# Kernel optimization log

Hardware: AMD Instinct MI355X
Metric: run time of the kernel (lower is better)

## Reference

```python
import jax, jax.numpy as jnp
import numpy as np

B, S, D, H = 4, 2048, 1024, 16
DK = D // H

def setup_inputs() -> dict:
    key = jax.random.key(0)
    ks = jax.random.split(key, 8)
    q = jax.random.normal(ks[0], (B, S, D), dtype=jnp.float32)
    k = jax.random.normal(ks[1], (B, S, D), dtype=jnp.float32)
    v = jax.random.normal(ks[2], (B, S, D), dtype=jnp.float32)
    # broadcastable causal mask [1,1,S,S]; 0 -> masked
    mask = jnp.tril(jnp.ones((S, S), dtype=jnp.int32))[None, None]
    sc = 1.0 / np.sqrt(D)
    w_q = jax.random.normal(ks[3], (D, D), dtype=jnp.float32) * sc
    w_k = jax.random.normal(ks[4], (D, D), dtype=jnp.float32) * sc
    w_v = jax.random.normal(ks[5], (D, D), dtype=jnp.float32) * sc
    w_o = jax.random.normal(ks[6], (D, D), dtype=jnp.float32) * sc
    return {"q": q, "k": k, "v": v, "mask": mask,
            "w_q": w_q, "w_k": w_k, "w_v": w_v, "w_o": w_o}


def reference(q, k, v, mask, w_q, w_k, w_v, w_o):
    # Linear (no bias): x @ W^T, torch convention
    def proj(x, w):
        return jnp.einsum('bsd,ed->bse', x, w)
    # [B,S,D] -> [B,H,S,DK]
    def split_heads(x):
        return x.reshape(B, S, H, DK).transpose(0, 2, 1, 3)

    query = split_heads(proj(q, w_q))
    key_ = split_heads(proj(k, w_k))
    value = split_heads(proj(v, w_v))

    scores = jnp.einsum('bhqd,bhkd->bhqk', query, key_) / jnp.sqrt(
        jnp.asarray(DK, dtype=query.dtype))
    scores = jnp.where(mask == 0, jnp.asarray(-1e9, dtype=scores.dtype), scores)
    attn = jax.nn.softmax(scores, axis=-1)  # dropout p=0.0 -> identity
    x = jnp.einsum('bhqk,bhkd->bhqd', attn, value)
    x = x.transpose(0, 2, 1, 3).reshape(B, S, D)
    return jnp.einsum('bsd,ed->bse', x, w_o)
```

## Files before the change

kernel.cpp:

```cpp
#include <hip/hip_runtime.h>
#include <hip/hip_bf16.h>

#define B_ 4
#define S_ 2048
#define D_ 1024
#define H_ 16
#define DK_ 64

typedef unsigned short u16;
typedef __bf16 bf16x8 __attribute__((ext_vector_type(8)));
typedef float f32x4 __attribute__((ext_vector_type(4)));

typedef const unsigned int __attribute__((address_space(1))) guint;
typedef unsigned int __attribute__((address_space(3))) luint;

__device__ __forceinline__ void gld16(const u16* g, u16* l) {
  __builtin_amdgcn_global_load_lds((guint*)g, (luint*)l, 16, 0, 0);
}

__device__ __forceinline__ u16 f2b(float f) {
  __hip_bfloat16 h = __float2bfloat16(f);
  return __builtin_bit_cast(u16, h);
}
__device__ __forceinline__ ushort4 f2b4(float4 f) {
  ushort4 r;
  r.x = f2b(f.x); r.y = f2b(f.y); r.z = f2b(f.z); r.w = f2b(f.w);
  return r;
}
__device__ __forceinline__ bf16x8 ldb8(const u16* p) {
  union { uint4 u; bf16x8 v; } x;
  x.u = *(const uint4*)p;
  return x.v;
}

struct CvtAllArgs {
  const float* s[7];
  u16* d[7];
};
__global__ __launch_bounds__(256) void cvt_all(CvtAllArgs a) {
  const int z = blockIdx.y;
  const int bx = blockIdx.x;
  const float* s;
  u16* d;
  int i;
  if (z < 3) {
    s = a.s[z]; d = a.d[z];
    i = bx * 256 + threadIdx.x;
  } else {
    if (bx >= 2048) return;
    const int wsel = bx >> 9;
    s = a.s[3 + wsel]; d = a.d[3 + wsel];
    i = (bx & 511) * 256 + threadIdx.x;
  }
  float4 x = ((const float4*)s)[2 * i];
  float4 y = ((const float4*)s)[2 * i + 1];
  ((ushort4*)d)[2 * i] = f2b4(x);
  ((ushort4*)d)[2 * i + 1] = f2b4(y);
}

__device__ __forceinline__ void swz_bnbm(int& bn, int& bm) {
  const int id2 = blockIdx.y * 8 + blockIdx.x;
  const int wg = (id2 & 7) * 64 + (id2 >> 3);
  bn = wg & 7;
  bm = wg >> 3;
}

template <bool OUT_QKV>
__device__ __forceinline__ void gemm_body(const u16* __restrict__ A,
                                          const u16* __restrict__ W,
                                          void* __restrict__ C, float scale) {
  constexpr int K = D_;
  __shared__ u16 As[128 * 32];
  __shared__ u16 Ws[128 * 32];
  const int t = threadIdx.x;
  const int lane = t & 63, w = t >> 6;
  const int quad = lane >> 4, m16 = lane & 15;
  int bn, bm;
  swz_bnbm(bn, bm);
  const int wm = (w >> 1) * 64, wn = (w & 1) * 64;
  const int sr = lane >> 2, sc8 = (lane & 3) * 8;

  f32x4 acc[4][4];
  const f32x4 zero = {0.f, 0.f, 0.f, 0.f};
#pragma unroll
  for (int i = 0; i < 4; i++)
#pragma unroll
    for (int j = 0; j < 4; j++) acc[i][j] = zero;

  const u16* Ag = A + (size_t)(bm * 128 + w * 32 + sr) * K + sc8;
  const u16* Wg = W + (size_t)(bn * 128 + w * 32 + sr) * K + sc8;
  u16* AsB = &As[w * 1024];
  u16* WsB = &Ws[w * 1024];

  for (int k0 = 0; k0 < K; k0 += 32) {
    __syncthreads();
    gld16(Ag + k0, AsB);
    gld16(Ag + (size_t)16 * K + k0, AsB + 512);
    gld16(Wg + k0, WsB);
    gld16(Wg + (size_t)16 * K + k0, WsB + 512);
    __syncthreads();

    bf16x8 af[4], wf[4];
#pragma unroll
    for (int mt = 0; mt < 4; mt++)
      af[mt] = ldb8(&As[(wm + mt * 16 + m16) * 32 + quad * 8]);
#pragma unroll
    for (int nt = 0; nt < 4; nt++)
      wf[nt] = ldb8(&Ws[(wn + nt * 16 + m16) * 32 + quad * 8]);
#pragma unroll
    for (int mt = 0; mt < 4; mt++)
#pragma unroll
      for (int nt = 0; nt < 4; nt++)
        acc[mt][nt] = __builtin_amdgcn_mfma_f32_16x16x32_bf16(af[mt], wf[nt],
                                                              acc[mt][nt], 0, 0, 0);
  }

#pragma unroll
  for (int mt = 0; mt < 4; mt++) {
#pragma unroll
    for (int r = 0; r < 4; r++) {
      int m = bm * 128 + wm + mt * 16 + quad * 4 + r;
#pragma unroll
      for (int nt = 0; nt < 4; nt++) {
        int n = bn * 128 + wn + nt * 16 + m16;
        float val = acc[mt][nt][r] * scale;
        if (OUT_QKV) {
          int b = m >> 11, s = m & (S_ - 1);
          int h = n >> 6, dk = n & 63;
          ((u16*)C)[(((size_t)b * H_ + h) * S_ + s) * DK_ + dk] = f2b(val);
        } else {
          ((float*)C)[(size_t)m * D_ + n] = val;
        }
      }
    }
  }
}

struct GemmQkvArgs {
  const u16 *a0, *a1, *a2;
  const u16 *w0, *w1, *w2;
  u16 *c0, *c1, *c2;
  float qscale;
};
__global__ __launch_bounds__(256) void gemm_qkv(GemmQkvArgs g) {
  const int z = blockIdx.z;
  const u16* A = z == 0 ? g.a0 : z == 1 ? g.a1 : g.a2;
  const u16* W = z == 0 ? g.w0 : z == 1 ? g.w1 : g.w2;
  u16* C = z == 0 ? g.c0 : z == 1 ? g.c1 : g.c2;
  gemm_body<true>(A, W, C, z == 0 ? g.qscale : 1.0f);
}

__global__ __launch_bounds__(256) void gemm_o(const u16* __restrict__ A,
                                              const u16* __restrict__ W,
                                              float* __restrict__ C) {
  gemm_body<false>(A, W, C, 1.0f);
}

__global__ __launch_bounds__(256) void transpose_v(const u16* __restrict__ Vp,
                                                   u16* __restrict__ VpT) {
  constexpr int LDT = 72;
  __shared__ u16 T[64 * LDT];
  const int t = threadIdx.x;
  const int s0 = blockIdx.x * 64, bh = blockIdx.y;
  const size_t base = (size_t)bh * S_ * DK_;
  const int rot = t & 7;
#pragma unroll
  for (int i = 0; i < 2; i++) {
    int c = t + i * 256, row = c >> 3, c8 = (c & 7) * 8;
    union { uint4 u; u16 s[8]; } uv;
    uv.u = *(const uint4*)(Vp + base + (size_t)(s0 + row) * DK_ + c8);
#pragma unroll
    for (int j0 = 0; j0 < 8; j0++) {
      int j = (j0 + rot) & 7;
      T[(c8 + j) * LDT + row] = uv.s[j];
    }
  }
  __syncthreads();
#pragma unroll
  for (int i = 0; i < 2; i++) {
    int c = t + i * 256, row = c >> 3, c8 = (c & 7) * 8;
    uint4 val = *(const uint4*)&T[row * LDT + c8];
    *(uint4*)(VpT + base + (size_t)row * S_ + s0 + c8) = val;
  }
}

__global__ __launch_bounds__(512, 4) void flash_attn(const u16* __restrict__ Qp,
                                                     const u16* __restrict__ Kp,
                                                     const u16* __restrict__ VpT,
                                                     u16* __restrict__ Xb) {
  constexpr int LDK = 72;
  __shared__ u16 Ks[2][64 * LDK];
  __shared__ u16 Vt[2][64 * LDK];
  __shared__ u16 Ps[8][16 * LDK];
  const int t = threadIdx.x;
  const int lane = t & 63, w = t >> 6;
  const int quad = lane >> 4, m16 = lane & 15;
  const int id = blockIdx.x;
  const int g = (id >> 3) & 7;
  const int bh = (id & 7) * 8 + (id >> 6);
  const int b = bh >> 4, h = bh & (H_ - 1);
  const size_t base = (size_t)bh * S_ * DK_;
  const int srow = t >> 3, sc8 = (t & 7) * 8;
  const f32x4 zero = {0.f, 0.f, 0.f, 0.f};

#pragma unroll 1
  for (int pi = 0; pi < 2; pi++) {
    const int qt = pi ? (15 - g) : g;
    const int q0 = qt * 128;
    const int nT = 2 * qt + 2;

    const int qrow = q0 + w * 16 + m16;
    bf16x8 qf0 = ldb8(Qp + base + (size_t)qrow * DK_ + quad * 8);
    bf16x8 qf1 = ldb8(Qp + base + (size_t)qrow * DK_ + 32 + quad * 8);

    f32x4 acc[4];
#pragma unroll
    for (int i = 0; i < 4; i++) acc[i] = zero;
    float rsum[4] = {0.f, 0.f, 0.f, 0.f};

    uint4 kr = *(const uint4*)(Kp + base + (size_t)srow * DK_ + sc8);
    uint4 vr = *(const uint4*)(VpT + base + (size_t)srow * S_ + sc8);

#pragma unroll 1
    for (int ti = 0; ti < nT; ti++) {
      const int kt0 = ti * 64;
      const int cur = ti & 1;
      *(uint4*)&Ks[cur][srow * LDK + sc8] = kr;
      *(uint4*)&Vt[cur][srow * LDK + sc8] = vr;
      __syncthreads();
      if (ti + 1 < nT) {
        kr = *(const uint4*)(Kp + base + (size_t)(kt0 + 64 + srow) * DK_ + sc8);
        vr = *(const uint4*)(VpT + base + (size_t)srow * S_ + kt0 + 64 + sc8);
      }
      const u16* Kc = Ks[cur];
      const u16* Vc = Vt[cur];

      f32x4 sc[4];
      __builtin_amdgcn_s_setprio(1);
#pragma unroll
      for (int nt = 0; nt < 4; nt++) {
        bf16x8 kf0 = ldb8(&Kc[(nt * 16 + m16) * LDK + quad * 8]);
        bf16x8 kf1 = ldb8(&Kc[(nt * 16 + m16) * LDK + 32 + quad * 8]);
        sc[nt] = __builtin_amdgcn_mfma_f32_16x16x32_bf16(kf0, qf0, zero, 0, 0, 0);
        sc[nt] = __builtin_amdgcn_mfma_f32_16x16x32_bf16(kf1, qf1, sc[nt], 0, 0, 0);
      }
      __builtin_amdgcn_s_setprio(0);

      if (ti >= nT - 2) {
        const int qcol = q0 + w * 16 + m16;
#pragma unroll
        for (int nt = 0; nt < 4; nt++) {
          int kg = kt0 + nt * 16 + quad * 4;
#pragma unroll
          for (int r = 0; r < 4; r++)
            if (kg + r > qcol) sc[nt][r] = -1e30f;
        }
      }

      u16* Pw = &Ps[w][0];
#pragma unroll
      for (int nt = 0; nt < 4; nt++) {
        ushort4 pk;
        float p0 = __builtin_amdgcn_exp2f(sc[nt][0]);
        float p1 = __builtin_amdgcn_exp2f(sc[nt][1]);
        float p2 = __builtin_amdgcn_exp2f(sc[nt][2]);
        float p3 = __builtin_amdgcn_exp2f(sc[nt][3]);
        rsum[nt] += (p0 + p1) + (p2 + p3);
        pk.x = f2b(p0); pk.y = f2b(p1); pk.z = f2b(p2); pk.w = f2b(p3);
        *(ushort4*)&Pw[m16 * LDK + nt * 16 + quad * 4] = pk;
      }

      __builtin_amdgcn_s_setprio(1);
#pragma unroll
      for (int s2 = 0; s2 < 2; s2++) {
        bf16x8 pf = ldb8(&Pw[m16 * LDK + s2 * 32 + quad * 8]);
#pragma unroll
        for (int nt = 0; nt < 4; nt++) {
          bf16x8 vf = ldb8(&Vc[(nt * 16 + m16) * LDK + s2 * 32 + quad * 8]);
          acc[nt] = __builtin_amdgcn_mfma_f32_16x16x32_bf16(pf, vf, acc[nt], 0, 0, 0);
        }
      }
      __builtin_amdgcn_s_setprio(0);
    }

    float tot = (rsum[0] + rsum[1]) + (rsum[2] + rsum[3]);
    tot += __shfl_xor(tot, 16);
    tot += __shfl_xor(tot, 32);
    float rcv[4];
#pragma unroll
    for (int r = 0; r < 4; r++)
      rcv[r] = __builtin_amdgcn_rcpf(__shfl(tot, quad * 4 + r, 16));
#pragma unroll
    for (int nt = 0; nt < 4; nt++)
#pragma unroll
      for (int r = 0; r < 4; r++) {
        int rg = q0 + w * 16 + quad * 4 + r;
        Xb[((size_t)b * S_ + rg) * D_ + h * DK_ + nt * 16 + m16] =
            f2b(acc[nt][r] * rcv[r]);
      }
  }
}

extern "C" void kernel_launch(void* const* d_in, const int* in_sizes, int n_in,
                              void* d_out, int out_size, void* d_ws, size_t ws_size,
                              hipStream_t stream) {
  (void)in_sizes; (void)n_in; (void)out_size; (void)ws_size;
  const float* q = (const float*)d_in[0];
  const float* k = (const float*)d_in[1];
  const float* v = (const float*)d_in[2];
  const float* wq = (const float*)d_in[4];
  const float* wk = (const float*)d_in[5];
  const float* wv = (const float*)d_in[6];
  const float* wo = (const float*)d_in[7];

  const size_t nBSD = (size_t)B_ * S_ * D_;
  const size_t nDD = (size_t)D_ * D_;
  u16* ab = (u16*)d_ws;
  u16* wqb = ab + nBSD;
  u16* wkb = wqb + nDD;
  u16* wvb = wkb + nDD;
  u16* wob = wvb + nDD;
  u16* Qp = wob + nDD;
  u16* Kp = Qp + nBSD;
  u16* Vp = Kp + nBSD;
  u16* VpT = ab;
  u16* Xb = Vp;
  u16* abk = (u16*)d_out;
  u16* abv = abk + nBSD;

  const float qscale = 0.125f * 1.44269504089f;

  CvtAllArgs ca = {{q, k, v, wq, wk, wv, wo}, {ab, abk, abv, wqb, wkb, wvb, wob}};
  cvt_all<<<dim3(nBSD / 2048, 4), 256, 0, stream>>>(ca);

  GemmQkvArgs gq = {ab, abk, abv, wqb, wkb, wvb, Qp, Kp, Vp, qscale};
  gemm_qkv<<<dim3(D_ / 128, (B_ * S_) / 128, 3), 256, 0, stream>>>(gq);

  transpose_v<<<dim3(S_ / 64, B_ * H_), 256, 0, stream>>>(Vp, VpT);
  flash_attn<<<512, 512, 0, stream>>>(Qp, Kp, VpT, Xb);

  gemm_o<<<dim3(D_ / 128, (B_ * S_) / 128), 256, 0, stream>>>(Xb, wob, (float*)d_out);
}
```

Measured before the change: 326.8 us.

## Rewrite projection GEMMs as 128x256 tiles with double-buffered LDS; split attention blocks

The projection and output GEMMs become 512-thread kernels with 128x256 tiles, a BK=64 double-buffered LDS pipeline using direct global-to-LDS loads, XOR swizzling and explicit vmcnt waits and barriers. This targets the low reuse and exposed load latency of the old 128x128, BK=32 loop, which synchronised twice per step. Flash attention now runs one query tile per block over 1024 blocks, longest tiles first, with a swizzled P buffer and a higher occupancy hint. The hand-written wait counts and barriers are fragile, and the larger tiles launch fewer blocks.

```diff
diff --git a/kernel.cpp b/kernel.cpp
--- a/kernel.cpp
+++ b/kernel.cpp
@@ -58,27 +58,58 @@
   ((ushort4*)d)[2 * i + 1] = f2b4(y);
 }
 
-__device__ __forceinline__ void swz_bnbm(int& bn, int& bm) {
-  const int id2 = blockIdx.y * 8 + blockIdx.x;
-  const int wg = (id2 & 7) * 64 + (id2 >> 3);
-  bn = wg & 7;
-  bm = wg >> 3;
-}
+#define PRIO1 __builtin_amdgcn_s_setprio(1)
+#define PRIO0 __builtin_amdgcn_s_setprio(0)
+#define BAR __builtin_amdgcn_s_barrier()
+
+#define STG_A(b, tt)                                                          \
+  do {                                                                        \
+    gld16(Ag + (size_t)(tt) * 64, &As[(b) * 8192 + w * 512]);                 \
+    gld16(Ag + (size_t)64 * K + (tt) * 64, &As[(b) * 8192 + 4096 + w * 512]); \
+  } while (0)
+#define STG_B(b, tt)                                                          \
+  do {                                                                        \
+    gld16(Wg + (size_t)(tt) * 64, &Bs[(b) * 16384 + w * 512]);                \
+    gld16(Wg + (size_t)64 * K + (tt) * 64, &Bs[(b) * 16384 + 4096 + w * 512]);\
+    gld16(Wg + (size_t)128 * K + (tt) * 64, &Bs[(b) * 16384 + 8192 + w * 512]);\
+    gld16(Wg + (size_t)192 * K + (tt) * 64, &Bs[(b) * 16384 + 12288 + w * 512]);\
+  } while (0)
+#define MM_HALF(mlo)                                                          \
+  do {                                                                        \
+    _Pragma("unroll") for (int mi_ = (mlo); mi_ < (mlo) + 2; mi_++)           \
+        _Pragma("unroll") for (int ni_ = 0; ni_ < 4; ni_++)                   \
+            _Pragma("unroll") for (int ks_ = 0; ks_ < 2; ks_++)               \
+                acc[mi_][ni_] = __builtin_amdgcn_mfma_f32_16x16x32_bf16(      \
+                    aA[mi_ * 2 + ks_], bB[ni_ * 2 + ks_], acc[mi_][ni_], 0, 0, 0); \
+  } while (0)
 
 template <bool OUT_QKV>
-__device__ __forceinline__ void gemm_body(const u16* __restrict__ A,
-                                          const u16* __restrict__ W,
-                                          void* __restrict__ C, float scale) {
+__device__ __forceinline__ void gemm4_body(const u16* __restrict__ A,
+                                           const u16* __restrict__ W,
+                                           void* __restrict__ C, float scale,
+                                           int bm, int bn) {
   constexpr int K = D_;
-  __shared__ u16 As[128 * 32];
-  __shared__ u16 Ws[128 * 32];
+  constexpr int NI = 8;
+  __shared__ u16 As[2 * 8192];
+  __shared__ u16 Bs[2 * 16384];
   const int t = threadIdx.x;
-  const int lane = t & 63, w = t >> 6;
-  const int quad = lane >> 4, m16 = lane & 15;
-  int bn, bm;
-  swz_bnbm(bn, bm);
-  const int wm = (w >> 1) * 64, wn = (w & 1) * 64;
-  const int sr = lane >> 2, sc8 = (lane & 3) * 8;
+  const int l = t & 63, w = t >> 6;
+  const int quad = l >> 4, m16 = l & 15;
+  const int wm = w >> 2, wn = w & 3;
+  const int lr = l >> 3;
+  const int swz = (m16 & 7) << 3;
+
+  const u16* Ag = A + (size_t)(bm * 128 + w * 8 + lr) * K + ((l & 7) ^ lr) * 8;
+  const u16* Wg = W + (size_t)(bn * 256 + w * 8 + lr) * K + ((l & 7) ^ lr) * 8;
+
+  int au[8], bu[8];
+#pragma unroll
+  for (int i = 0; i < 4; i++)
+#pragma unroll
+    for (int ks = 0; ks < 2; ks++) {
+      au[i * 2 + ks] = ((wm * 64 + i * 16 + m16) * 64 + ks * 32 + quad * 8) ^ swz;
+      bu[i * 2 + ks] = ((wn * 64 + i * 16 + m16) * 64 + ks * 32 + quad * 8) ^ swz;
+    }
 
   f32x4 acc[4][4];
   const f32x4 zero = {0.f, 0.f, 0.f, 0.f};
@@ -87,43 +118,52 @@
 #pragma unroll
     for (int j = 0; j < 4; j++) acc[i][j] = zero;
 
-  const u16* Ag = A + (size_t)(bm * 128 + w * 32 + sr) * K + sc8;
-  const u16* Wg = W + (size_t)(bn * 128 + w * 32 + sr) * K + sc8;
-  u16* AsB = &As[w * 1024];
-  u16* WsB = &Ws[w * 1024];
-
-  for (int k0 = 0; k0 < K; k0 += 32) {
-    __syncthreads();
-    gld16(Ag + k0, AsB);
-    gld16(Ag + (size_t)16 * K + k0, AsB + 512);
-    gld16(Wg + k0, WsB);
-    gld16(Wg + (size_t)16 * K + k0, WsB + 512);
-    __syncthreads();
-
-    bf16x8 af[4], wf[4];
-#pragma unroll
-    for (int mt = 0; mt < 4; mt++)
-      af[mt] = ldb8(&As[(wm + mt * 16 + m16) * 32 + quad * 8]);
-#pragma unroll
-    for (int nt = 0; nt < 4; nt++)
-      wf[nt] = ldb8(&Ws[(wn + nt * 16 + m16) * 32 + quad * 8]);
-#pragma unroll
-    for (int mt = 0; mt < 4; mt++)
-#pragma unroll
-      for (int nt = 0; nt < 4; nt++)
-        acc[mt][nt] = __builtin_amdgcn_mfma_f32_16x16x32_bf16(af[mt], wf[nt],
-                                                              acc[mt][nt], 0, 0, 0);
-  }
-
-#pragma unroll
-  for (int mt = 0; mt < 4; mt++) {
+  bf16x8 aA[8], bB[8];
+
+  STG_A(0, 0); STG_B(0, 0);
+  STG_A(1, 1); STG_B(1, 1);
+  asm volatile("s_waitcnt vmcnt(6)" ::: "memory");
+  __builtin_amdgcn_sched_barrier(0);
+  BAR;
+
+#pragma unroll 1
+  for (int j = 0; j < NI; j++) {
+    const bool st = (j + 1 < NI);
+#pragma unroll
+    for (int i = 0; i < 8; i++) aA[i] = ldb8(&As[au[i]]);
+#pragma unroll
+    for (int i = 0; i < 8; i++) bB[i] = ldb8(&Bs[bu[i]]);
+    BAR; PRIO1; MM_HALF(0); PRIO0; BAR;
+    if (st) {
+      STG_A(0, 2 * j + 2); STG_B(0, 2 * j + 2);
+      asm volatile("s_waitcnt vmcnt(6)" ::: "memory");
+    } else {
+      asm volatile("s_waitcnt vmcnt(0)" ::: "memory");
+    }
+    __builtin_amdgcn_sched_barrier(0);
+    BAR; PRIO1; MM_HALF(2); PRIO0; BAR;
+#pragma unroll
+    for (int i = 0; i < 8; i++) aA[i] = ldb8(&As[8192 + au[i]]);
+#pragma unroll
+    for (int i = 0; i < 8; i++) bB[i] = ldb8(&Bs[16384 + bu[i]]);
+    BAR; PRIO1; MM_HALF(0); PRIO0; BAR;
+    if (st) {
+      STG_A(1, 2 * j + 3); STG_B(1, 2 * j + 3);
+      asm volatile("s_waitcnt vmcnt(6)" ::: "memory");
+    }
+    __builtin_amdgcn_sched_barrier(0);
+    BAR; PRIO1; MM_HALF(2); PRIO0; BAR;
+  }
+
+#pragma unroll
+  for (int mi = 0; mi < 4; mi++) {
 #pragma unroll
     for (int r = 0; r < 4; r++) {
-      int m = bm * 128 + wm + mt * 16 + quad * 4 + r;
-#pragma unroll
-      for (int nt = 0; nt < 4; nt++) {
-        int n = bn * 128 + wn + nt * 16 + m16;
-        float val = acc[mt][nt][r] * scale;
+      int m = bm * 128 + wm * 64 + mi * 16 + quad * 4 + r;
+#pragma unroll
+      for (int ni = 0; ni < 4; ni++) {
+        int n = bn * 256 + wn * 64 + ni * 16 + m16;
+        float val = acc[mi][ni][r] * scale;
         if (OUT_QKV) {
           int b = m >> 11, s = m & (S_ - 1);
           int h = n >> 6, dk = n & 63;
@@ -142,18 +182,24 @@
   u16 *c0, *c1, *c2;
   float qscale;
 };
-__global__ __launch_bounds__(256) void gemm_qkv(GemmQkvArgs g) {
-  const int z = blockIdx.z;
-  const u16* A = z == 0 ? g.a0 : z == 1 ? g.a1 : g.a2;
-  const u16* W = z == 0 ? g.w0 : z == 1 ? g.w1 : g.w2;
-  u16* C = z == 0 ? g.c0 : z == 1 ? g.c1 : g.c2;
-  gemm_body<true>(A, W, C, z == 0 ? g.qscale : 1.0f);
-}
-
-__global__ __launch_bounds__(256) void gemm_o(const u16* __restrict__ A,
-                                              const u16* __restrict__ W,
-                                              float* __restrict__ C) {
-  gemm_body<false>(A, W, C, 1.0f);
+__global__ __launch_bounds__(512, 2) void gemm_qkv4(GemmQkvArgs g) {
+  const int id3 = (blockIdx.z * 64 + blockIdx.y) * 4 + blockIdx.x;
+  const int wg = (id3 & 7) * 96 + (id3 >> 3);
+  const int zz = wg >> 8, rem = wg & 255;
+  const int bm = rem >> 2, bn = rem & 3;
+  const u16* A = zz == 0 ? g.a0 : zz == 1 ? g.a1 : g.a2;
+  const u16* W = zz == 0 ? g.w0 : zz == 1 ? g.w1 : g.w2;
+  u16* C = zz == 0 ? g.c0 : zz == 1 ? g.c1 : g.c2;
+  gemm4_body<true>(A, W, C, zz == 0 ? g.qscale : 1.0f, bm, bn);
+}
+
+__global__ __launch_bounds__(512, 2) void gemm_o(const u16* __restrict__ A,
+                                                 const u16* __restrict__ W,
+                                                 float* __restrict__ C) {
+  const int id2 = blockIdx.y * 4 + blockIdx.x;
+  const int wg = (id2 & 7) * 32 + (id2 >> 3);
+  const int bm = wg >> 2, bn = wg & 3;
+  gemm4_body<false>(A, W, C, 1.0f, bm, bn);
 }
 
 __global__ __launch_bounds__(256) void transpose_v(const u16* __restrict__ Vp,
@@ -184,121 +230,118 @@
   }
 }
 
-__global__ __launch_bounds__(512, 4) void flash_attn(const u16* __restrict__ Qp,
+__global__ __launch_bounds__(512, 6) void flash_attn(const u16* __restrict__ Qp,
                                                      const u16* __restrict__ Kp,
                                                      const u16* __restrict__ VpT,
                                                      u16* __restrict__ Xb) {
   constexpr int LDK = 72;
   __shared__ u16 Ks[2][64 * LDK];
   __shared__ u16 Vt[2][64 * LDK];
-  __shared__ u16 Ps[8][16 * LDK];
+  __shared__ u16 Ps[8][1024];
   const int t = threadIdx.x;
   const int lane = t & 63, w = t >> 6;
   const int quad = lane >> 4, m16 = lane & 15;
   const int id = blockIdx.x;
-  const int g = (id >> 3) & 7;
-  const int bh = (id & 7) * 8 + (id >> 6);
+  const int qt = 15 - (id >> 6);
+  const int bh = id & 63;
   const int b = bh >> 4, h = bh & (H_ - 1);
   const size_t base = (size_t)bh * S_ * DK_;
   const int srow = t >> 3, sc8 = (t & 7) * 8;
+  const int psw = (m16 & 7) << 3;
   const f32x4 zero = {0.f, 0.f, 0.f, 0.f};
 
+  const int q0 = qt * 128;
+  const int nT = 2 * qt + 2;
+
+  const int qrow = q0 + w * 16 + m16;
+  bf16x8 qf0 = ldb8(Qp + base + (size_t)qrow * DK_ + quad * 8);
+  bf16x8 qf1 = ldb8(Qp + base + (size_t)qrow * DK_ + 32 + quad * 8);
+
+  f32x4 acc[4];
+#pragma unroll
+  for (int i = 0; i < 4; i++) acc[i] = zero;
+  float rsum[4] = {0.f, 0.f, 0.f, 0.f};
+
+  uint4 kr = *(const uint4*)(Kp + base + (size_t)srow * DK_ + sc8);
+  uint4 vr = *(const uint4*)(VpT + base + (size_t)srow * S_ + sc8);
+
 #pragma unroll 1
-  for (int pi = 0; pi < 2; pi++) {
-    const int qt = pi ? (15 - g) : g;
-    const int q0 = qt * 128;
-    const int nT = 2 * qt + 2;
-
-    const int qrow = q0 + w * 16 + m16;
-    bf16x8 qf0 = ldb8(Qp + base + (size_t)qrow * DK_ + quad * 8);
-    bf16x8 qf1 = ldb8(Qp + base + (size_t)qrow * DK_ + 32 + quad * 8);
-
-    f32x4 acc[4];
-#pragma unroll
-    for (int i = 0; i < 4; i++) acc[i] = zero;
-    float rsum[4] = {0.f, 0.f, 0.f, 0.f};
-
-    uint4 kr = *(const uint4*)(Kp + base + (size_t)srow * DK_ + sc8);
-    uint4 vr = *(const uint4*)(VpT + base + (size_t)srow * S_ + sc8);
-
-#pragma unroll 1
-    for (int ti = 0; ti < nT; ti++) {
-      const int kt0 = ti * 64;
-      const int cur = ti & 1;
-      *(uint4*)&Ks[cur][srow * LDK + sc8] = kr;
-      *(uint4*)&Vt[cur][srow * LDK + sc8] = vr;
-      __syncthreads();
-      if (ti + 1 < nT) {
-        kr = *(const uint4*)(Kp + base + (size_t)(kt0 + 64 + srow) * DK_ + sc8);
-        vr = *(const uint4*)(VpT + base + (size_t)srow * S_ + kt0 + 64 + sc8);
+  for (int ti = 0; ti < nT; ti++) {
+    const int kt0 = ti * 64;
+    const int cur = ti & 1;
+    *(uint4*)&Ks[cur][srow * LDK + sc8] = kr;
+    *(uint4*)&Vt[cur][srow * LDK + sc8] = vr;
+    __syncthreads();
+    if (ti + 1 < nT) {
+      kr = *(const uint4*)(Kp + base + (size_t)(kt0 + 64 + srow) * DK_ + sc8);
+      vr = *(const uint4*)(VpT + base + (size_t)srow * S_ + kt0 + 64 + sc8);
+    }
+    const u16* Kc = Ks[cur];
+    const u16* Vc = Vt[cur];
+
+    f32x4 sc[4];
+    __builtin_amdgcn_s_setprio(1);
+#pragma unroll
+    for (int nt = 0; nt < 4; nt++) {
+      bf16x8 kf0 = ldb8(&Kc[(nt * 16 + m16) * LDK + quad * 8]);
+      bf16x8 kf1 = ldb8(&Kc[(nt * 16 + m16) * LDK + 32 + quad * 8]);
+      sc[nt] = __builtin_amdgcn_mfma_f32_16x16x32_bf16(kf0, qf0, zero, 0, 0, 0);
+      sc[nt] = __builtin_amdgcn_mfma_f32_16x16x32_bf16(kf1, qf1, sc[nt], 0, 0, 0);
+    }
+    __builtin_amdgcn_s_setprio(0);
+
+    if (ti >= nT - 2) {
+      const int qcol = q0 + w * 16 + m16;
+#pragma unroll
+      for (int nt = 0; nt < 4; nt++) {
+        int kg = kt0 + nt * 16 + quad * 4;
+#pragma unroll
+        for (int r = 0; r < 4; r++)
+          if (kg + r > qcol) sc[nt][r] = -1e30f;
       }
-      const u16* Kc = Ks[cur];
-      const u16* Vc = Vt[cur];
-
-      f32x4 sc[4];
-      __builtin_amdgcn_s_setprio(1);
+    }
+
+    u16* Pw = &Ps[w][0];
+#pragma unroll
+    for (int nt = 0; nt < 4; nt++) {
+      ushort4 pk;
+      float p0 = __builtin_amdgcn_exp2f(sc[nt][0]);
+      float p1 = __builtin_amdgcn_exp2f(sc[nt][1]);
+      float p2 = __builtin_amdgcn_exp2f(sc[nt][2]);
+      float p3 = __builtin_amdgcn_exp2f(sc[nt][3]);
+      rsum[nt] += (p0 + p1) + (p2 + p3);
+      pk.x = f2b(p0); pk.y = f2b(p1); pk.z = f2b(p2); pk.w = f2b(p3);
+      *(ushort4*)&Pw[(m16 * 64 + nt * 16 + quad * 4) ^ psw] = pk;
+    }
+
+    __builtin_amdgcn_s_setprio(1);
+#pragma unroll
+    for (int s2 = 0; s2 < 2; s2++) {
+      bf16x8 pf = ldb8(&Pw[(m16 * 64 + s2 * 32 + quad * 8) ^ psw]);
 #pragma unroll
       for (int nt = 0; nt < 4; nt++) {
-        bf16x8 kf0 = ldb8(&Kc[(nt * 16 + m16) * LDK + quad * 8]);
-        bf16x8 kf1 = ldb8(&Kc[(nt * 16 + m16) * LDK + 32 + quad * 8]);
-        sc[nt] = __builtin_amdgcn_mfma_f32_16x16x32_bf16(kf0, qf0, zero, 0, 0, 0);
-        sc[nt] = __builtin_amdgcn_mfma_f32_16x16x32_bf16(kf1, qf1, sc[nt], 0, 0, 0);
+        bf16x8 vf = ldb8(&Vc[(nt * 16 + m16) * LDK + s2 * 32 + quad * 8]);
+        acc[nt] = __builtin_amdgcn_mfma_f32_16x16x32_bf16(pf, vf, acc[nt], 0, 0, 0);
       }
-      __builtin_amdgcn_s_setprio(0);
-
-      if (ti >= nT - 2) {
-        const int qcol = q0 + w * 16 + m16;
-#pragma unroll
-        for (int nt = 0; nt < 4; nt++) {
-          int kg = kt0 + nt * 16 + quad * 4;
-#pragma unroll
-          for (int r = 0; r < 4; r++)
-            if (kg + r > qcol) sc[nt][r] = -1e30f;
-        }
-      }
-
-      u16* Pw = &Ps[w][0];
-#pragma unroll
-      for (int nt = 0; nt < 4; nt++) {
-        ushort4 pk;
-        float p0 = __builtin_amdgcn_exp2f(sc[nt][0]);
-        float p1 = __builtin_amdgcn_exp2f(sc[nt][1]);
-        float p2 = __builtin_amdgcn_exp2f(sc[nt][2]);
-        float p3 = __builtin_amdgcn_exp2f(sc[nt][3]);
-        rsum[nt] += (p0 + p1) + (p2 + p3);
-        pk.x = f2b(p0); pk.y = f2b(p1); pk.z = f2b(p2); pk.w = f2b(p3);
-        *(ushort4*)&Pw[m16 * LDK + nt * 16 + quad * 4] = pk;
-      }
-
-      __builtin_amdgcn_s_setprio(1);
-#pragma unroll
-      for (int s2 = 0; s2 < 2; s2++) {
-        bf16x8 pf = ldb8(&Pw[m16 * LDK + s2 * 32 + quad * 8]);
-#pragma unroll
-        for (int nt = 0; nt < 4; nt++) {
-          bf16x8 vf = ldb8(&Vc[(nt * 16 + m16) * LDK + s2 * 32 + quad * 8]);
-          acc[nt] = __builtin_amdgcn_mfma_f32_16x16x32_bf16(pf, vf, acc[nt], 0, 0, 0);
-        }
-      }
-      __builtin_amdgcn_s_setprio(0);
-    }
-
-    float tot = (rsum[0] + rsum[1]) + (rsum[2] + rsum[3]);
-    tot += __shfl_xor(tot, 16);
-    tot += __shfl_xor(tot, 32);
-    float rcv[4];
-#pragma unroll
-    for (int r = 0; r < 4; r++)
-      rcv[r] = __builtin_amdgcn_rcpf(__shfl(tot, quad * 4 + r, 16));
-#pragma unroll
-    for (int nt = 0; nt < 4; nt++)
-#pragma unroll
-      for (int r = 0; r < 4; r++) {
-        int rg = q0 + w * 16 + quad * 4 + r;
-        Xb[((size_t)b * S_ + rg) * D_ + h * DK_ + nt * 16 + m16] =
-            f2b(acc[nt][r] * rcv[r]);
-      }
-  }
+    }
+    __builtin_amdgcn_s_setprio(0);
+  }
+
+  float tot = (rsum[0] + rsum[1]) + (rsum[2] + rsum[3]);
+  tot += __shfl_xor(tot, 16);
+  tot += __shfl_xor(tot, 32);
+  float rcv[4];
+#pragma unroll
+  for (int r = 0; r < 4; r++)
+    rcv[r] = __builtin_amdgcn_rcpf(__shfl(tot, quad * 4 + r, 16));
+#pragma unroll
+  for (int nt = 0; nt < 4; nt++)
+#pragma unroll
+    for (int r = 0; r < 4; r++) {
+      int rg = q0 + w * 16 + quad * 4 + r;
+      Xb[((size_t)b * S_ + rg) * D_ + h * DK_ + nt * 16 + m16] =
+          f2b(acc[nt][r] * rcv[r]);
+    }
 }
 
 extern "C" void kernel_launch(void* const* d_in, const int* in_sizes, int n_in,
@@ -334,10 +377,10 @@
   cvt_all<<<dim3(nBSD / 2048, 4), 256, 0, stream>>>(ca);
 
   GemmQkvArgs gq = {ab, abk, abv, wqb, wkb, wvb, Qp, Kp, Vp, qscale};
-  gemm_qkv<<<dim3(D_ / 128, (B_ * S_) / 128, 3), 256, 0, stream>>>(gq);
+  gemm_qkv4<<<dim3(4, 64, 3), 512, 0, stream>>>(gq);
 
   transpose_v<<<dim3(S_ / 64, B_ * H_), 256, 0, stream>>>(Vp, VpT);
-  flash_attn<<<512, 512, 0, stream>>>(Qp, Kp, VpT, Xb);
-
-  gemm_o<<<dim3(D_ / 128, (B_ * S_) / 128), 256, 0, stream>>>(Xb, wob, (float*)d_out);
-}
+  flash_attn<<<1024, 512, 0, stream>>>(Qp, Kp, VpT, Xb);
+
+  gemm_o<<<dim3(4, 64), 512, 0, stream>>>(Xb, wob, (float*)d_out);
+}
```

New measurement: 321.9 us. No clear change (-1.5%).
